# Optimization experiments

Measured on AMD Instinct MI355X. Metric: run time of the kernel, lower is better.

## Reference

```python
import jax, jax.numpy as jnp
import numpy as np

DIM = 1024
CTX_DIM = 1024
VALUE_DIM = 1024
HEADS = 16
HEAD_DIM = DIM // HEADS        # q/k head dim = 64
V_HEAD_DIM = VALUE_DIM // HEADS
LN_EPS = 1e-5


def setup_inputs() -> dict:
    key = jax.random.key(0)
    k0, k1, k2, k3, k4 = jax.random.split(key, 5)
    B, N, M = 4, 1024, 1024
    x = jax.random.normal(k0, (B, N, DIM), jnp.float32)
    context = jax.random.normal(k1, (B, M, CTX_DIM), jnp.float32)
    # Linear weights stored as [in, out] (y = x @ W), matching torch Linear math
    Wq = jax.random.normal(k2, (DIM, DIM), jnp.float32) * (DIM ** -0.5)
    Wkv = jax.random.normal(k3, (CTX_DIM, DIM + VALUE_DIM), jnp.float32) * (CTX_DIM ** -0.5)
    Wt = jax.random.normal(k4, (HEADS, HEADS), jnp.float32) * (HEADS ** -0.5)
    gamma = jnp.ones((HEADS,), jnp.float32)
    beta = jnp.zeros((HEADS,), jnp.float32)
    return {"x": x, "context": context, "Wq": Wq, "Wkv": Wkv,
            "Wt": Wt, "gamma": gamma, "beta": beta}


def reference(x, context, Wq, Wkv, Wt, gamma, beta):
    B, N, _ = x.shape
    M = context.shape[1]
    # projections
    q = (x @ Wq).reshape(B, N, HEADS, HEAD_DIM).transpose(0, 2, 1, 3)       # [B,H,N,d]
    kv = context @ Wkv                                                      # [B,M,dim+vdim]
    k = kv[..., :DIM].reshape(B, M, HEADS, HEAD_DIM).transpose(0, 2, 1, 3)  # [B,H,M,d]
    v = kv[..., DIM:].reshape(B, M, HEADS, V_HEAD_DIM).transpose(0, 2, 1, 3)
    # scaled dot-product scores, fully materialized as in the original
    scale = HEAD_DIM ** -0.5
    dots = jnp.einsum('bhid,bhjd->bhij', q * scale, k)                      # [B,H,N,M]
    w = jax.nn.softmax(dots, axis=-1)
    # talking heads: Linear(heads,heads,bias=False) then LayerNorm(heads) over head axis
    w = jnp.einsum('bhij,hg->bgij', w, Wt)
    mu = jnp.mean(w, axis=1, keepdims=True)
    var = jnp.var(w, axis=1, keepdims=True)
    w = (w - mu) * jax.lax.rsqrt(var + LN_EPS)
    w = w * gamma[None, :, None, None] + beta[None, :, None, None]
    attn = jnp.einsum('bhij,bhjd->bhid', w, v)                              # [B,H,N,vd]
    out = attn.transpose(0, 2, 1, 3).reshape(B, N, VALUE_DIM)
    return out
```

## Files before the change

kernel.cpp:

```cpp
#include <hip/hip_runtime.h>
#include <hip/hip_bf16.h>

typedef __bf16 bf16;
typedef bf16 bf16x2 __attribute__((ext_vector_type(2)));
typedef bf16 bf16x4 __attribute__((ext_vector_type(4)));
typedef bf16 bf16x8 __attribute__((ext_vector_type(8)));
typedef float floatx4 __attribute__((ext_vector_type(4)));

#define MFMA_BF16(a, b, c) __builtin_amdgcn_mfma_f32_16x16x32_bf16((a), (b), (c), 0, 0, 0)

__global__ __launch_bounds__(256) void cvt_kernel(const float* __restrict__ in,
                                                  bf16* __restrict__ out, int n8) {
    int idx = blockIdx.x * 256 + threadIdx.x;
    if (idx >= n8) return;
    const float* src = in + (size_t)idx * 8;
    float4 f0 = *(const float4*)src;
    float4 f1 = *(const float4*)(src + 4);
    bf16x8 v = {(bf16)f0.x, (bf16)f0.y, (bf16)f0.z, (bf16)f0.w,
                (bf16)f1.x, (bf16)f1.y, (bf16)f1.z, (bf16)f1.w};
    *(bf16x8*)(out + (size_t)idx * 8) = v;
}

__global__ __launch_bounds__(256) void trans_kernel(const float* __restrict__ in,
                                                    bf16* __restrict__ out, int R, int C) {
    __shared__ float tile[32][33];
    const int t = threadIdx.x;
    const int r0 = blockIdx.y * 32, c0 = blockIdx.x * 32;
    int r = t >> 3, c4 = (t & 7) * 4;
    float4 v = *(const float4*)&in[(size_t)(r0 + r) * C + c0 + c4];
    tile[r][c4 + 0] = v.x; tile[r][c4 + 1] = v.y;
    tile[r][c4 + 2] = v.z; tile[r][c4 + 3] = v.w;
    __syncthreads();
    int rp = t >> 3, cp = (t & 7) * 4;
    bf16x4 w = {(bf16)tile[cp + 0][rp], (bf16)tile[cp + 1][rp],
                (bf16)tile[cp + 2][rp], (bf16)tile[cp + 3][rp]};
    *(bf16x4*)&out[(size_t)(c0 + rp) * R + r0 + cp] = w;
}

__global__ __launch_bounds__(256) void vtrans_kernel(const bf16* __restrict__ in,
                                                     bf16* __restrict__ out) {
    __shared__ bf16 tile[32][36];
    const int t = threadIdx.x;
    const int r0 = blockIdx.y * 32, c0 = blockIdx.x * 32;
    int r = t >> 3, c4 = (t & 7) * 4;
    bf16x4 v = *(const bf16x4*)&in[(size_t)(r0 + r) * 1024 + c0 + c4];
    tile[r][c4 + 0] = v[0]; tile[r][c4 + 1] = v[1];
    tile[r][c4 + 2] = v[2]; tile[r][c4 + 3] = v[3];
    __syncthreads();
    int rp = t >> 3, cp = (t & 7) * 4;
    int hd = c0 + rp;
    int b = r0 >> 10, j = (r0 & 1023) + cp;
    bf16x4 w = {tile[cp + 0][rp], tile[cp + 1][rp], tile[cp + 2][rp], tile[cp + 3][rp]};
    *(bf16x4*)&out[(size_t)(b * 1024 + hd) * 1024 + j] = w;
}

template <int MODE>
__global__ __launch_bounds__(256) void gemm128(const bf16* __restrict__ A,
                                               const bf16* __restrict__ B,
                                               bf16* __restrict__ C,
                                               bf16* __restrict__ V, int N) {
    __shared__ bf16 As[128 * 40];
    __shared__ bf16 Bs[128 * 40];
    const int t = threadIdx.x;
    const int wv = t >> 6, lane = t & 63, quad = lane >> 4, l15 = lane & 15;
    const int wr = wv >> 1, wc = wv & 1;
    const int m0 = blockIdx.y * 128, n0 = blockIdx.x * 128;
    const int ra = t >> 1, kc = (t & 1) * 16;

    floatx4 acc[4][4] = {};

    for (int k0 = 0; k0 < 1024; k0 += 32) {
        bf16x8 a0 = *(const bf16x8*)&A[(size_t)(m0 + ra) * 1024 + k0 + kc];
        bf16x8 a1 = *(const bf16x8*)&A[(size_t)(m0 + ra) * 1024 + k0 + kc + 8];
        bf16x8 b0 = *(const bf16x8*)&B[(size_t)(n0 + ra) * 1024 + k0 + kc];
        bf16x8 b1 = *(const bf16x8*)&B[(size_t)(n0 + ra) * 1024 + k0 + kc + 8];
        __syncthreads();
        *(bf16x8*)&As[ra * 40 + kc] = a0;
        *(bf16x8*)&As[ra * 40 + kc + 8] = a1;
        *(bf16x8*)&Bs[ra * 40 + kc] = b0;
        *(bf16x8*)&Bs[ra * 40 + kc + 8] = b1;
        __syncthreads();
        bf16x8 af[4], bfr[4];
#pragma unroll
        for (int mt = 0; mt < 4; ++mt)
            af[mt] = *(bf16x8*)&As[(wr * 64 + mt * 16 + l15) * 40 + quad * 8];
#pragma unroll
        for (int nt = 0; nt < 4; ++nt)
            bfr[nt] = *(bf16x8*)&Bs[(wc * 64 + nt * 16 + l15) * 40 + quad * 8];
#pragma unroll
        for (int mt = 0; mt < 4; ++mt)
#pragma unroll
            for (int nt = 0; nt < 4; ++nt)
                acc[mt][nt] = MFMA_BF16(af[mt], bfr[nt], acc[mt][nt]);
    }
#pragma unroll
    for (int mt = 0; mt < 4; ++mt)
#pragma unroll
        for (int nt = 0; nt < 4; ++nt)
#pragma unroll
            for (int r = 0; r < 4; ++r) {
                int m = m0 + wr * 64 + mt * 16 + quad * 4 + r;
                int n = n0 + wc * 64 + nt * 16 + l15;
                bf16 val = (bf16)acc[mt][nt][r];
                if (MODE == 0) {
                    C[(size_t)m * N + n] = val;
                } else {
                    if (n < 1024) C[(size_t)m * 1024 + n] = val;
                    else          V[(size_t)m * 1024 + (n - 1024)] = val;
                }
            }
}

__global__ __launch_bounds__(256) void denom_kernel(const bf16* __restrict__ Qb,
                                                    const bf16* __restrict__ Kb,
                                                    float* __restrict__ L) {
    const int t = threadIdx.x;
    const int wv = t >> 6, lane = t & 63, quad = lane >> 4, l15 = lane & 15;
    const int i0 = blockIdx.x * 32, b = blockIdx.y, jz = blockIdx.z;
    const float scale = 0.125f;

    bf16x8 qa[4][2][2];
#pragma unroll
    for (int hh = 0; hh < 4; ++hh)
#pragma unroll
        for (int it = 0; it < 2; ++it) {
            const bf16* qp = Qb + (size_t)(b * 1024 + i0 + it * 16 + l15) * 1024 +
                             (wv * 4 + hh) * 64 + quad * 8;
            qa[hh][it][0] = *(const bf16x8*)qp;
            qa[hh][it][1] = *(const bf16x8*)(qp + 32);
        }
    floatx4 se[4][2] = {};
    const bf16* Kbase = Kb + (size_t)b * 1024 * 1024;

    for (int jt = 0; jt < 16; ++jt) {
        int j = jz * 256 + jt * 16 + l15;
#pragma unroll
        for (int hh = 0; hh < 4; ++hh) {
            const bf16* kp = Kbase + (size_t)j * 1024 + (wv * 4 + hh) * 64 + quad * 8;
            bf16x8 k0 = *(const bf16x8*)kp;
            bf16x8 k1 = *(const bf16x8*)(kp + 32);
#pragma unroll
            for (int it = 0; it < 2; ++it) {
                floatx4 c = {0.f, 0.f, 0.f, 0.f};
                c = MFMA_BF16(qa[hh][it][0], k0, c);
                c = MFMA_BF16(qa[hh][it][1], k1, c);
#pragma unroll
                for (int r = 0; r < 4; ++r) se[hh][it][r] += __expf(c[r] * scale);
            }
        }
    }
#pragma unroll
    for (int hh = 0; hh < 4; ++hh)
#pragma unroll
        for (int it = 0; it < 2; ++it)
#pragma unroll
            for (int r = 0; r < 4; ++r) {
                float s = se[hh][it][r];
                s += __shfl_xor(s, 1); s += __shfl_xor(s, 2);
                s += __shfl_xor(s, 4); s += __shfl_xor(s, 8);
                if (l15 == 0)
                    atomicAdd(&L[(size_t)(b * 16 + wv * 4 + hh) * 1024 + i0 + it * 16 +
                                 quad * 4 + r], s);
            }
}

__global__ __launch_bounds__(512, 4) void attn_kernel(const bf16* __restrict__ Qb,
                                                      const bf16* __restrict__ Kb,
                                                      const bf16* __restrict__ Vt,
                                                      const float* __restrict__ L,
                                                      const float* __restrict__ Wt,
                                                      const float* __restrict__ gamma,
                                                      const float* __restrict__ beta,
                                                      float* __restrict__ out) {
    __shared__ bf16 Buf1[512 * 20];
    __shared__ bf16 Buf2[16 * 648];
    __shared__ __align__(16) bf16 Zbuf[8];

    const int t = threadIdx.x;
    const int wv = t >> 6, lane = t & 63, quad = lane >> 4, l15 = lane & 15;
    const int i0 = blockIdx.x * 16, b = blockIdx.y, jz = blockIdx.z;
    const float scale = 0.125f;

    if (t < 8) Zbuf[t] = (bf16)0.f;

    bf16x8 a_wt;
#pragma unroll
    for (int jj = 0; jj < 8; ++jj) {
        int k = quad * 8 + jj;
        float v = 0.f;
        if (k < 16) {
            float s = 0.f;
            for (int g = 0; g < 16; ++g) s += Wt[k * 16 + g];
            v = Wt[k * 16 + l15] - s * 0.0625f;
        }
        a_wt[jj] = (bf16)v;
    }
    float gq[4], bq[4];
#pragma unroll
    for (int r = 0; r < 4; ++r) { gq[r] = gamma[quad * 4 + r]; bq[r] = beta[quad * 4 + r]; }

    bf16x8 qa[2][2];
    float invl[2][4];
#pragma unroll
    for (int hh = 0; hh < 2; ++hh) {
        int h = wv * 2 + hh;
        const bf16* qp = Qb + (size_t)(b * 1024 + i0 + l15) * 1024 + h * 64 + quad * 8;
        qa[hh][0] = *(const bf16x8*)qp;
        qa[hh][1] = *(const bf16x8*)(qp + 32);
#pragma unroll
        for (int r = 0; r < 4; ++r)
            invl[hh][r] = 1.f / L[(size_t)(b * 16 + h) * 1024 + i0 + quad * 4 + r];
    }

    const bf16* Kbase = Kb + (size_t)b * 1024 * 1024;
    const bf16* Vbase = Vt + (size_t)b * 16 * 64 * 1024;
    floatx4 o[2][4] = {};

    for (int jt = 0; jt < 16; ++jt) {
        const int j0 = jz * 512 + jt * 32;
#pragma unroll
        for (int ns = 0; ns < 2; ++ns) {
            floatx4 cw[2];
#pragma unroll
            for (int hh = 0; hh < 2; ++hh) {
                int h = wv * 2 + hh;
                const bf16* kp = Kbase + (size_t)(j0 + ns * 16 + l15) * 1024 + h * 64 + quad * 8;
                floatx4 c = {0.f, 0.f, 0.f, 0.f};
                c = MFMA_BF16(qa[hh][0], *(const bf16x8*)kp, c);
                c = MFMA_BF16(qa[hh][1], *(const bf16x8*)(kp + 32), c);
                cw[hh] = c;
            }
#pragma unroll
            for (int r = 0; r < 4; ++r) {
                bf16x2 pk = {(bf16)(__expf(cw[0][r] * scale) * invl[0][r]),
                             (bf16)(__expf(cw[1][r] * scale) * invl[1][r])};
                *(bf16x2*)&Buf1[((quad * 4 + r) * 32 + ns * 16 + l15) * 20 + wv * 2] = pk;
            }
        }
        __syncthreads();
#pragma unroll
        for (int grp = 0; grp < 4; ++grp) {
            int gi = wv * 4 + grp, ig = gi >> 1, jb = (gi & 1) * 16;
            int p = ig * 32 + jb + l15;
            const bf16* src = (quad < 2) ? &Buf1[p * 20 + quad * 8] : Zbuf;
            floatx4 c = {0.f, 0.f, 0.f, 0.f};
            c = MFMA_BF16(a_wt, *(const bf16x8*)src, c);
            float s2 = c[0] * c[0] + c[1] * c[1] + c[2] * c[2] + c[3] * c[3];
            s2 += __shfl_xor(s2, 16);
            s2 += __shfl_xor(s2, 32);
            float rs = rsqrtf(s2 * 0.0625f + 1e-5f);
#pragma unroll
            for (int r = 0; r < 4; ++r) {
                float w2 = c[r] * rs * gq[r] + bq[r];
                Buf2[(quad * 4 + r) * 648 + ig * 40 + jb + l15] = (bf16)w2;
            }
        }
        __syncthreads();
#pragma unroll
        for (int hh = 0; hh < 2; ++hh) {
            int g = wv * 2 + hh;
            bf16x8 a = *(bf16x8*)&Buf2[g * 648 + l15 * 40 + quad * 8];
#pragma unroll
            for (int dt = 0; dt < 4; ++dt) {
                const bf16* vp = Vbase + (size_t)(g * 64 + dt * 16 + l15) * 1024 + j0 + quad * 8;
                o[hh][dt] = MFMA_BF16(a, *(const bf16x8*)vp, o[hh][dt]);
            }
        }
    }
#pragma unroll
    for (int hh = 0; hh < 2; ++hh) {
        int g = wv * 2 + hh;
#pragma unroll
        for (int dt = 0; dt < 4; ++dt)
#pragma unroll
            for (int r = 0; r < 4; ++r)
                atomicAdd(&out[(size_t)(b * 1024 + i0 + quad * 4 + r) * 1024 +
                               g * 64 + dt * 16 + l15], o[hh][dt][r]);
    }
}

extern "C" void kernel_launch(void* const* d_in, const int* in_sizes, int n_in,
                              void* d_out, int out_size, void* d_ws, size_t ws_size,
                              hipStream_t stream) {
    const float* x     = (const float*)d_in[0];
    const float* ctx   = (const float*)d_in[1];
    const float* Wq    = (const float*)d_in[2];
    const float* Wkv   = (const float*)d_in[3];
    const float* Wt    = (const float*)d_in[4];
    const float* gamma = (const float*)d_in[5];
    const float* beta  = (const float*)d_in[6];
    float* out = (float*)d_out;

    bf16* xb   = (bf16*)d_ws;
    bf16* cb   = xb + (size_t)4 * 1024 * 1024;
    bf16* WqT  = cb + (size_t)4 * 1024 * 1024;
    bf16* WkvT = WqT + (size_t)1024 * 1024;
    bf16* Qb   = WkvT + (size_t)2048 * 1024;
    bf16* Kb   = Qb + (size_t)4 * 1024 * 1024;
    bf16* Vr   = Kb + (size_t)4 * 1024 * 1024;
    bf16* Vt   = Vr + (size_t)4 * 1024 * 1024;
    float* L   = (float*)(Vt + (size_t)4 * 1024 * 1024);

    hipMemsetAsync(L, 0, (size_t)4 * 16 * 1024 * sizeof(float), stream);
    hipMemsetAsync(out, 0, (size_t)out_size * sizeof(float), stream);

    cvt_kernel<<<2048, 256, 0, stream>>>(x, xb, 524288);
    cvt_kernel<<<2048, 256, 0, stream>>>(ctx, cb, 524288);
    trans_kernel<<<dim3(32, 32), 256, 0, stream>>>(Wq, WqT, 1024, 1024);
    trans_kernel<<<dim3(64, 32), 256, 0, stream>>>(Wkv, WkvT, 1024, 2048);

    gemm128<0><<<dim3(8, 32), 256, 0, stream>>>(xb, WqT, Qb, nullptr, 1024);
    gemm128<1><<<dim3(16, 32), 256, 0, stream>>>(cb, WkvT, Kb, Vr, 2048);
    vtrans_kernel<<<dim3(32, 128), 256, 0, stream>>>(Vr, Vt);

    denom_kernel<<<dim3(32, 4, 4), 256, 0, stream>>>(Qb, Kb, L);
    attn_kernel<<<dim3(64, 4, 2), 512, 0, stream>>>(Qb, Kb, Vt, L, Wt, gamma, beta, out);
}
```

Measured before the change: 356.2 us.

## Merge prep kernels, fuse V transpose into GEMM, widen attention j-tile

Merges the two conversion launches and the two weight-transpose launches into single launches. Combines the Q and KV projection GEMMs into one grid and has the GEMM write V directly in transposed layout, which removes the separate V transpose kernel and its buffer. Splits the denominator kernel over twice as many j-chunks for more parallelism and sets an occupancy hint on it. Doubles the attention inner tile from 32 to 64 keys per iteration with larger shared buffers, halving the number of barriers per block at the cost of more LDS per block.

```diff
diff --git a/kernel.cpp b/kernel.cpp
--- a/kernel.cpp
+++ b/kernel.cpp
@@ -9,20 +9,33 @@
 
 #define MFMA_BF16(a, b, c) __builtin_amdgcn_mfma_f32_16x16x32_bf16((a), (b), (c), 0, 0, 0)
 
-__global__ __launch_bounds__(256) void cvt_kernel(const float* __restrict__ in,
-                                                  bf16* __restrict__ out, int n8) {
+__global__ __launch_bounds__(256) void cvt2_kernel(const float* __restrict__ x,
+                                                   const float* __restrict__ ctx,
+                                                   bf16* __restrict__ xb,
+                                                   bf16* __restrict__ cb) {
     int idx = blockIdx.x * 256 + threadIdx.x;
-    if (idx >= n8) return;
-    const float* src = in + (size_t)idx * 8;
+    const float* in;
+    bf16* out;
+    int i;
+    if (idx < 524288) { in = x; out = xb; i = idx; }
+    else              { in = ctx; out = cb; i = idx - 524288; }
+    const float* src = in + (size_t)i * 8;
     float4 f0 = *(const float4*)src;
     float4 f1 = *(const float4*)(src + 4);
     bf16x8 v = {(bf16)f0.x, (bf16)f0.y, (bf16)f0.z, (bf16)f0.w,
                 (bf16)f1.x, (bf16)f1.y, (bf16)f1.z, (bf16)f1.w};
-    *(bf16x8*)(out + (size_t)idx * 8) = v;
-}
-
-__global__ __launch_bounds__(256) void trans_kernel(const float* __restrict__ in,
-                                                    bf16* __restrict__ out, int R, int C) {
+    *(bf16x8*)(out + (size_t)i * 8) = v;
+}
+
+__global__ __launch_bounds__(256) void trans2_kernel(const float* __restrict__ Wq,
+                                                     const float* __restrict__ Wkv,
+                                                     bf16* __restrict__ WqT,
+                                                     bf16* __restrict__ WkvT) {
+    const int z = blockIdx.z;
+    if (z == 0 && blockIdx.x >= 32) return;
+    const float* in = z ? Wkv : Wq;
+    bf16* out = z ? WkvT : WqT;
+    const int C = z ? 2048 : 1024, R = 1024;
     __shared__ float tile[32][33];
     const int t = threadIdx.x;
     const int r0 = blockIdx.y * 32, c0 = blockIdx.x * 32;
@@ -37,34 +50,23 @@
     *(bf16x4*)&out[(size_t)(c0 + rp) * R + r0 + cp] = w;
 }
 
-__global__ __launch_bounds__(256) void vtrans_kernel(const bf16* __restrict__ in,
-                                                     bf16* __restrict__ out) {
-    __shared__ bf16 tile[32][36];
-    const int t = threadIdx.x;
-    const int r0 = blockIdx.y * 32, c0 = blockIdx.x * 32;
-    int r = t >> 3, c4 = (t & 7) * 4;
-    bf16x4 v = *(const bf16x4*)&in[(size_t)(r0 + r) * 1024 + c0 + c4];
-    tile[r][c4 + 0] = v[0]; tile[r][c4 + 1] = v[1];
-    tile[r][c4 + 2] = v[2]; tile[r][c4 + 3] = v[3];
-    __syncthreads();
-    int rp = t >> 3, cp = (t & 7) * 4;
-    int hd = c0 + rp;
-    int b = r0 >> 10, j = (r0 & 1023) + cp;
-    bf16x4 w = {tile[cp + 0][rp], tile[cp + 1][rp], tile[cp + 2][rp], tile[cp + 3][rp]};
-    *(bf16x4*)&out[(size_t)(b * 1024 + hd) * 1024 + j] = w;
-}
-
-template <int MODE>
-__global__ __launch_bounds__(256) void gemm128(const bf16* __restrict__ A,
-                                               const bf16* __restrict__ B,
-                                               bf16* __restrict__ C,
-                                               bf16* __restrict__ V, int N) {
+__global__ __launch_bounds__(256) void gemm_all(const bf16* __restrict__ xb,
+                                                const bf16* __restrict__ cb,
+                                                const bf16* __restrict__ WqT,
+                                                const bf16* __restrict__ WkvT,
+                                                bf16* __restrict__ Qb,
+                                                bf16* __restrict__ Kb,
+                                                bf16* __restrict__ Vt) {
     __shared__ bf16 As[128 * 40];
     __shared__ bf16 Bs[128 * 40];
+    const bool isQ = blockIdx.x < 8;
+    const bf16* A = isQ ? xb : cb;
+    const bf16* B = isQ ? WqT : WkvT;
     const int t = threadIdx.x;
     const int wv = t >> 6, lane = t & 63, quad = lane >> 4, l15 = lane & 15;
     const int wr = wv >> 1, wc = wv & 1;
-    const int m0 = blockIdx.y * 128, n0 = blockIdx.x * 128;
+    const int m0 = blockIdx.y * 128;
+    const int n0 = (isQ ? blockIdx.x : blockIdx.x - 8) * 128;
     const int ra = t >> 1, kc = (t & 1) * 16;
 
     floatx4 acc[4][4] = {};
@@ -96,24 +98,30 @@
 #pragma unroll
     for (int mt = 0; mt < 4; ++mt)
 #pragma unroll
-        for (int nt = 0; nt < 4; ++nt)
-#pragma unroll
-            for (int r = 0; r < 4; ++r) {
-                int m = m0 + wr * 64 + mt * 16 + quad * 4 + r;
-                int n = n0 + wc * 64 + nt * 16 + l15;
-                bf16 val = (bf16)acc[mt][nt][r];
-                if (MODE == 0) {
-                    C[(size_t)m * N + n] = val;
-                } else {
-                    if (n < 1024) C[(size_t)m * 1024 + n] = val;
-                    else          V[(size_t)m * 1024 + (n - 1024)] = val;
-                }
-            }
-}
-
-__global__ __launch_bounds__(256) void denom_kernel(const bf16* __restrict__ Qb,
-                                                    const bf16* __restrict__ Kb,
-                                                    float* __restrict__ L) {
+        for (int nt = 0; nt < 4; ++nt) {
+            int mb = m0 + wr * 64 + mt * 16 + quad * 4;
+            int n = n0 + wc * 64 + nt * 16 + l15;
+            if (isQ) {
+#pragma unroll
+                for (int r = 0; r < 4; ++r)
+                    Qb[(size_t)(mb + r) * 1024 + n] = (bf16)acc[mt][nt][r];
+            } else if (n < 1024) {
+#pragma unroll
+                for (int r = 0; r < 4; ++r)
+                    Kb[(size_t)(mb + r) * 1024 + n] = (bf16)acc[mt][nt][r];
+            } else {
+                int nn = n - 1024, h = nn >> 6, d = nn & 63;
+                int bb = mb >> 10, j = mb & 1023;
+                bf16x4 v4 = {(bf16)acc[mt][nt][0], (bf16)acc[mt][nt][1],
+                             (bf16)acc[mt][nt][2], (bf16)acc[mt][nt][3]};
+                *(bf16x4*)&Vt[(size_t)((bb * 16 + h) * 64 + d) * 1024 + j] = v4;
+            }
+        }
+}
+
+__global__ __launch_bounds__(256, 4) void denom_kernel(const bf16* __restrict__ Qb,
+                                                       const bf16* __restrict__ Kb,
+                                                       float* __restrict__ L) {
     const int t = threadIdx.x;
     const int wv = t >> 6, lane = t & 63, quad = lane >> 4, l15 = lane & 15;
     const int i0 = blockIdx.x * 32, b = blockIdx.y, jz = blockIdx.z;
@@ -132,8 +140,8 @@
     floatx4 se[4][2] = {};
     const bf16* Kbase = Kb + (size_t)b * 1024 * 1024;
 
-    for (int jt = 0; jt < 16; ++jt) {
-        int j = jz * 256 + jt * 16 + l15;
+    for (int jt = 0; jt < 8; ++jt) {
+        int j = jz * 128 + jt * 16 + l15;
 #pragma unroll
         for (int hh = 0; hh < 4; ++hh) {
             const bf16* kp = Kbase + (size_t)j * 1024 + (wv * 4 + hh) * 64 + quad * 8;
@@ -172,8 +180,8 @@
                                                       const float* __restrict__ gamma,
                                                       const float* __restrict__ beta,
                                                       float* __restrict__ out) {
-    __shared__ bf16 Buf1[512 * 20];
-    __shared__ bf16 Buf2[16 * 648];
+    __shared__ bf16 Buf1[1024 * 20];
+    __shared__ bf16 Buf2[16 * 1160];
     __shared__ __align__(16) bf16 Zbuf[8];
 
     const int t = threadIdx.x;
@@ -216,10 +224,10 @@
     const bf16* Vbase = Vt + (size_t)b * 16 * 64 * 1024;
     floatx4 o[2][4] = {};
 
-    for (int jt = 0; jt < 16; ++jt) {
-        const int j0 = jz * 512 + jt * 32;
-#pragma unroll
-        for (int ns = 0; ns < 2; ++ns) {
+    for (int jt = 0; jt < 8; ++jt) {
+        const int j0 = jz * 512 + jt * 64;
+#pragma unroll
+        for (int ns = 0; ns < 4; ++ns) {
             floatx4 cw[2];
 #pragma unroll
             for (int hh = 0; hh < 2; ++hh) {
@@ -234,14 +242,14 @@
             for (int r = 0; r < 4; ++r) {
                 bf16x2 pk = {(bf16)(__expf(cw[0][r] * scale) * invl[0][r]),
                              (bf16)(__expf(cw[1][r] * scale) * invl[1][r])};
-                *(bf16x2*)&Buf1[((quad * 4 + r) * 32 + ns * 16 + l15) * 20 + wv * 2] = pk;
+                *(bf16x2*)&Buf1[((quad * 4 + r) * 64 + ns * 16 + l15) * 20 + wv * 2] = pk;
             }
         }
         __syncthreads();
 #pragma unroll
-        for (int grp = 0; grp < 4; ++grp) {
-            int gi = wv * 4 + grp, ig = gi >> 1, jb = (gi & 1) * 16;
-            int p = ig * 32 + jb + l15;
+        for (int grp = 0; grp < 8; ++grp) {
+            int gi = wv * 8 + grp, ig = gi >> 2, jb = (gi & 3) * 16;
+            int p = ig * 64 + jb + l15;
             const bf16* src = (quad < 2) ? &Buf1[p * 20 + quad * 8] : Zbuf;
             floatx4 c = {0.f, 0.f, 0.f, 0.f};
             c = MFMA_BF16(a_wt, *(const bf16x8*)src, c);
@@ -252,18 +260,22 @@
 #pragma unroll
             for (int r = 0; r < 4; ++r) {
                 float w2 = c[r] * rs * gq[r] + bq[r];
-                Buf2[(quad * 4 + r) * 648 + ig * 40 + jb + l15] = (bf16)w2;
+                Buf2[(quad * 4 + r) * 1160 + ig * 72 + jb + l15] = (bf16)w2;
             }
         }
         __syncthreads();
 #pragma unroll
         for (int hh = 0; hh < 2; ++hh) {
             int g = wv * 2 + hh;
-            bf16x8 a = *(bf16x8*)&Buf2[g * 648 + l15 * 40 + quad * 8];
-#pragma unroll
-            for (int dt = 0; dt < 4; ++dt) {
-                const bf16* vp = Vbase + (size_t)(g * 64 + dt * 16 + l15) * 1024 + j0 + quad * 8;
-                o[hh][dt] = MFMA_BF16(a, *(const bf16x8*)vp, o[hh][dt]);
+#pragma unroll
+            for (int sub = 0; sub < 2; ++sub) {
+                bf16x8 a = *(bf16x8*)&Buf2[g * 1160 + l15 * 72 + sub * 32 + quad * 8];
+#pragma unroll
+                for (int dt = 0; dt < 4; ++dt) {
+                    const bf16* vp = Vbase + (size_t)(g * 64 + dt * 16 + l15) * 1024 +
+                                     j0 + sub * 32 + quad * 8;
+                    o[hh][dt] = MFMA_BF16(a, *(const bf16x8*)vp, o[hh][dt]);
+                }
             }
         }
     }
@@ -297,22 +309,15 @@
     bf16* WkvT = WqT + (size_t)1024 * 1024;
     bf16* Qb   = WkvT + (size_t)2048 * 1024;
     bf16* Kb   = Qb + (size_t)4 * 1024 * 1024;
-    bf16* Vr   = Kb + (size_t)4 * 1024 * 1024;
-    bf16* Vt   = Vr + (size_t)4 * 1024 * 1024;
+    bf16* Vt   = Kb + (size_t)4 * 1024 * 1024;
     float* L   = (float*)(Vt + (size_t)4 * 1024 * 1024);
 
     hipMemsetAsync(L, 0, (size_t)4 * 16 * 1024 * sizeof(float), stream);
     hipMemsetAsync(out, 0, (size_t)out_size * sizeof(float), stream);
 
-    cvt_kernel<<<2048, 256, 0, stream>>>(x, xb, 524288);
-    cvt_kernel<<<2048, 256, 0, stream>>>(ctx, cb, 524288);
-    trans_kernel<<<dim3(32, 32), 256, 0, stream>>>(Wq, WqT, 1024, 1024);
-    trans_kernel<<<dim3(64, 32), 256, 0, stream>>>(Wkv, WkvT, 1024, 2048);
-
-    gemm128<0><<<dim3(8, 32), 256, 0, stream>>>(xb, WqT, Qb, nullptr, 1024);
-    gemm128<1><<<dim3(16, 32), 256, 0, stream>>>(cb, WkvT, Kb, Vr, 2048);
-    vtrans_kernel<<<dim3(32, 128), 256, 0, stream>>>(Vr, Vt);
-
-    denom_kernel<<<dim3(32, 4, 4), 256, 0, stream>>>(Qb, Kb, L);
+    cvt2_kernel<<<4096, 256, 0, stream>>>(x, ctx, xb, cb);
+    trans2_kernel<<<dim3(64, 32, 2), 256, 0, stream>>>(Wq, Wkv, WqT, WkvT);
+    gemm_all<<<dim3(24, 32), 256, 0, stream>>>(xb, cb, WqT, WkvT, Qb, Kb, Vt);
+    denom_kernel<<<dim3(32, 4, 8), 256, 0, stream>>>(Qb, Kb, L);
     attn_kernel<<<dim3(64, 4, 2), 512, 0, stream>>>(Qb, Kb, Vt, L, Wt, gamma, beta, out);
 }
```

Result: slower. 422.5 us (+18.6%).
